# Kernel tuning notes

Hardware: AMD Instinct MI355X
Metric: run time of the kernel (lower is better)

## Reference

```python
import jax, jax.numpy as jnp
import numpy as np

B, N, D, G = 32, 1024, 512, 32  # batch, set size, in_features, num_gaussians


def setup_inputs() -> dict:
    key = jax.random.key(0)
    k1, k2 = jax.random.split(key)
    minibatch = jax.random.normal(k1, (B, N, D), dtype=jnp.float32)
    # xavier_uniform for Linear(D -> G)
    limit = float(np.sqrt(6.0 / (D + G)))
    W_pi = jax.random.uniform(k2, (G, D), dtype=jnp.float32, minval=-limit, maxval=limit)
    b_pi = jnp.zeros((G,), dtype=jnp.float32)
    return {"minibatch": minibatch, "W_pi": W_pi, "b_pi": b_pi}


def reference(minibatch, W_pi, b_pi):
    d = minibatch.shape[-1]
    o = d // 2
    # mixture weights per (batch, sample): softmax over gaussian axis
    logits = jnp.einsum('bnd,gd->bng', minibatch, W_pi) + b_pi  # [B,N,G]
    pi = jax.nn.softmax(logits, axis=2)
    mu = minibatch[:, :, :o]        # [B,N,O]
    sigma = minibatch[:, :, -o:]    # [B,N,O]
    weights = jnp.mean(pi, axis=1)  # [B,G]
    denom = jnp.sum(pi, axis=1)     # [B,G]
    # weighted first moment -> locs (vectorized over all gaussians at once)
    m1 = jnp.einsum('bng,bno->bgo', pi, mu)                 # [B,G,O]
    locs = m1 / denom[:, :, None]                            # [B,G,O]
    # weighted E[mu^2 + sigma^2]; variance = E[mu^2+sigma^2] - locs^2
    # (identical math to sum(pi*((locs-mu)^2 + sigma^2))/sum(pi))
    m2 = jnp.einsum('bng,bno->bgo', pi, mu * mu + sigma * sigma)
    var = m2 / denom[:, :, None] - locs * locs
    scales = jnp.sqrt(jnp.maximum(var, 0.0))                 # [B,G,O]
    return weights, scales, locs
```

## Files before the change

### kernel.cpp

```cpp
#include <hip/hip_runtime.h>
#include <stdint.h>

#define B_ 32
#define N_ 1024
#define D_ 512
#define G_ 32

typedef __attribute__((ext_vector_type(8))) short short8;
typedef __attribute__((ext_vector_type(4))) float f32x4;

union U4S8 { uint4 u; short8 s; };

#define WS_M   524288
#define WS_DN  2621440

__device__ inline uint32_t pack_bf16x2(float a, float b) {
  uint32_t ua = __float_as_uint(a);
  uint32_t ub = __float_as_uint(b);
  ua += 0x7FFFu + ((ua >> 16) & 1u);
  ub += 0x7FFFu + ((ub >> 16) & 1u);
  return (ua >> 16) | (ub & 0xFFFF0000u);
}
__device__ inline uint16_t bf16r(float a) {
  uint32_t u = __float_as_uint(a);
  u += 0x7FFFu + ((u >> 16) & 1u);
  return (uint16_t)(u >> 16);
}

__global__ __launch_bounds__(512, 8) void mdn_k1(
    const float* __restrict__ x, const float* __restrict__ W,
    const float* __restrict__ bpi, float* ws)
{
  __shared__ uint32_t Xb[4096];
  __shared__ uint32_t Wb[2048];
  __shared__ float SP[64 * 36];
  __shared__ uint32_t SPTb[1024];
  __shared__ float wpart[8 * 32];
  __shared__ float bias_s[G_];

  const int t = threadIdx.x;
  const int bid = blockIdx.x;
  const int b = bid >> 4;
  const int n0 = (bid & 15) * 64;
  const int wave = t >> 6;
  const int lane = t & 63;
  const int Mt = wave >> 1;
  const int Nt = wave & 1;

  int xr[2], xd[2];
  #pragma unroll
  for (int p = 0; p < 2; ++p) {
    int st = (p * 512 + t) * 16;
    xr[p] = st >> 8;
    xd[p] = ((st & 255) ^ ((xr[p] & 7) << 4)) >> 1;
  }
  int wg, wd;
  { int st = t * 16; wg = st >> 8; wd = ((st & 255) ^ ((wg & 7) << 4)) >> 1; }

  const float* xbase = x + ((size_t)b * N_ + n0) * D_;

  float4 fx[2][2], fw[2];
  #pragma unroll
  for (int p = 0; p < 2; ++p) {
    const float* s = xbase + xr[p] * D_ + xd[p];
    fx[p][0] = *(const float4*)s; fx[p][1] = *(const float4*)(s + 4);
  }
  { const float* s = W + wg * D_ + wd;
    fw[0] = *(const float4*)s; fw[1] = *(const float4*)(s + 4); }

  if (t < G_) bias_s[t] = bpi[t];

  f32x4 acc = {0.f, 0.f, 0.f, 0.f};

  #pragma unroll
  for (int dc = 0; dc < 4; ++dc) {
    #pragma unroll
    for (int p = 0; p < 2; ++p) {
      uint4 v;
      v.x = pack_bf16x2(fx[p][0].x, fx[p][0].y); v.y = pack_bf16x2(fx[p][0].z, fx[p][0].w);
      v.z = pack_bf16x2(fx[p][1].x, fx[p][1].y); v.w = pack_bf16x2(fx[p][1].z, fx[p][1].w);
      *(uint4*)((char*)Xb + (p * 512 + t) * 16) = v;
    }
    {
      uint4 v;
      v.x = pack_bf16x2(fw[0].x, fw[0].y); v.y = pack_bf16x2(fw[0].z, fw[0].w);
      v.z = pack_bf16x2(fw[1].x, fw[1].y); v.w = pack_bf16x2(fw[1].z, fw[1].w);
      *(uint4*)((char*)Wb + t * 16) = v;
    }
    __syncthreads();
    if (dc < 3) {
      #pragma unroll
      for (int p = 0; p < 2; ++p) {
        const float* s = xbase + xr[p] * D_ + (dc + 1) * 128 + xd[p];
        fx[p][0] = *(const float4*)s; fx[p][1] = *(const float4*)(s + 4);
      }
      const float* s = W + wg * D_ + (dc + 1) * 128 + wd;
      fw[0] = *(const float4*)s; fw[1] = *(const float4*)(s + 4);
    }
    #pragma unroll
    for (int ks = 0; ks < 4; ++ks) {
      int rowx = Mt * 16 + (lane & 15);
      int bytex = rowx * 256 + (((ks * 64) + ((lane >> 4) * 16)) ^ ((rowx & 7) << 4));
      short8 afr = *(short8*)((char*)Xb + bytex);
      int g = Nt * 16 + (lane & 15);
      int bytew = g * 256 + (((ks * 64) + ((lane >> 4) * 16)) ^ ((g & 7) << 4));
      short8 bfr = *(short8*)((char*)Wb + bytew);
      acc = __builtin_amdgcn_mfma_f32_16x16x32_bf16(afr, bfr, acc, 0, 0, 0);
    }
    __syncthreads();
  }

  {
    int g = Nt * 16 + (lane & 15);
    float bs = bias_s[g];
    int rbase = Mt * 16 + (lane >> 4) * 4;
    #pragma unroll
    for (int j = 0; j < 4; ++j) SP[(rbase + j) * 36 + g] = acc[j] + bs;
  }
  __syncthreads();

  {
    int r = t >> 3, gq = t & 7;
    float4 v = *(float4*)(SP + r * 36 + gq * 4);
    float m = fmaxf(fmaxf(v.x, v.y), fmaxf(v.z, v.w));
    m = fmaxf(m, __shfl_xor(m, 1));
    m = fmaxf(m, __shfl_xor(m, 2));
    m = fmaxf(m, __shfl_xor(m, 4));
    v.x = __expf(v.x - m); v.y = __expf(v.y - m);
    v.z = __expf(v.z - m); v.w = __expf(v.w - m);
    float s = v.x + v.y + v.z + v.w;
    s += __shfl_xor(s, 1); s += __shfl_xor(s, 2); s += __shfl_xor(s, 4);
    float inv = 1.0f / s;
    v.x *= inv; v.y *= inv; v.z *= inv; v.w *= inv;
    uint16_t* sp16 = (uint16_t*)SPTb;
    sp16[(gq * 4 + 0) * 64 + r] = bf16r(v.x);
    sp16[(gq * 4 + 1) * 64 + r] = bf16r(v.y);
    sp16[(gq * 4 + 2) * 64 + r] = bf16r(v.z);
    sp16[(gq * 4 + 3) * 64 + r] = bf16r(v.w);
    #pragma unroll
    for (int msk = 8; msk <= 32; msk <<= 1) {
      v.x += __shfl_xor(v.x, msk); v.y += __shfl_xor(v.y, msk);
      v.z += __shfl_xor(v.z, msk); v.w += __shfl_xor(v.w, msk);
    }
    if (lane < 8) {
      wpart[wave * 32 + lane * 4 + 0] = v.x;
      wpart[wave * 32 + lane * 4 + 1] = v.y;
      wpart[wave * 32 + lane * 4 + 2] = v.z;
      wpart[wave * 32 + lane * 4 + 3] = v.w;
    }
  }
  __syncthreads();

  if (t < 256) {
    int g = t >> 3, s = t & 7;
    uint4 v = *(uint4*)(SPTb + g * 32 + s * 4);
    *(uint4*)((uint32_t*)ws + (size_t)(b * 32 + g) * 512 + (n0 >> 1) + s * 4) = v;
  }
  if (t < G_) {
    float ssum = 0.f;
    #pragma unroll
    for (int w = 0; w < 8; ++w) ssum += wpart[w * 32 + t];
    ws[WS_DN + bid * 32 + t] = ssum;
  }
}

__global__ __launch_bounds__(512, 8) void mdn_k2(
    const float* __restrict__ x, float* ws)
{
  __shared__ uint32_t PT[32 * 132];
  __shared__ uint32_t XT[32 * 132];

  const int t = threadIdx.x;
  const int bid = blockIdx.x;
  const int b = bid >> 4;
  const int kc = (bid >> 2) & 3;
  const int q = bid & 3;
  const int wave = t >> 6, lane = t & 63;
  const int ot = wave;
  const int n0 = kc * 256;

  const uint32_t* piT = (const uint32_t*)ws;
  const int pg = t >> 4, psl = t & 15;
  const uint32_t* pbase = piT + (size_t)(b * 32 + pg) * 512 + kc * 128;
  uint4 pv0 = *(const uint4*)(pbase + psl * 4);
  uint4 pv1 = *(const uint4*)(pbase + (psl + 16) * 4);

  const int r2l = t >> 4, c4 = t & 15;
  const float* xb2 = x + ((size_t)b * N_ + n0) * D_ + q * 64 + 4 * c4;
  float4 a0, a1, sv0, sv1;
  {
    const float* s = xb2 + (size_t)(2 * r2l) * D_;
    a0 = *(const float4*)s;        a1 = *(const float4*)(s + D_);
    sv0 = *(const float4*)(s + 256); sv1 = *(const float4*)(s + D_ + 256);
  }

  *(uint4*)(PT + pg * 132 + psl * 4) = pv0;
  *(uint4*)(PT + pg * 132 + (psl + 16) * 4) = pv1;
  __syncthreads();

  f32x4 acc[2] = {{0.f,0.f,0.f,0.f},{0.f,0.f,0.f,0.f}};

  #pragma unroll
  for (int sc = 0; sc < 4; ++sc) {
    {
      uint4 wmu, wm2;
      wmu.x = pack_bf16x2(a0.x, a1.x); wmu.y = pack_bf16x2(a0.y, a1.y);
      wmu.z = pack_bf16x2(a0.z, a1.z); wmu.w = pack_bf16x2(a0.w, a1.w);
      float4 u0 = make_float4(fmaf(a0.x, a0.x, sv0.x * sv0.x), fmaf(a0.y, a0.y, sv0.y * sv0.y),
                              fmaf(a0.z, a0.z, sv0.z * sv0.z), fmaf(a0.w, a0.w, sv0.w * sv0.w));
      float4 u1 = make_float4(fmaf(a1.x, a1.x, sv1.x * sv1.x), fmaf(a1.y, a1.y, sv1.y * sv1.y),
                              fmaf(a1.z, a1.z, sv1.z * sv1.z), fmaf(a1.w, a1.w, sv1.w * sv1.w));
      wm2.x = pack_bf16x2(u0.x, u1.x); wm2.y = pack_bf16x2(u0.y, u1.y);
      wm2.z = pack_bf16x2(u0.z, u1.z); wm2.w = pack_bf16x2(u0.w, u1.w);
      *(uint4*)(XT + r2l * 132 + 4 * c4) = wmu;
      *(uint4*)(XT + r2l * 132 + 64 + 4 * c4) = wm2;
    }
    __syncthreads();
    if (sc < 3) {
      const float* s = xb2 + (size_t)((sc + 1) * 64 + 2 * r2l) * D_;
      a0 = *(const float4*)s;        a1 = *(const float4*)(s + D_);
      sv0 = *(const float4*)(s + 256); sv1 = *(const float4*)(s + D_ + 256);
    }
    #pragma unroll
    for (int kl = 0; kl < 2; ++kl) {
      int rb = kl * 16 + (lane >> 4) * 4;
      int ol = ot * 16 + (lane & 15);
      U4S8 bf;
      bf.u.x = XT[(rb + 0) * 132 + ol];
      bf.u.y = XT[(rb + 1) * 132 + ol];
      bf.u.z = XT[(rb + 2) * 132 + ol];
      bf.u.w = XT[(rb + 3) * 132 + ol];
      int r0h = (sc * 2 + kl) * 16 + (lane >> 4) * 4;
      #pragma unroll
      for (int gt = 0; gt < 2; ++gt) {
        int ga = gt * 16 + (lane & 15);
        short8 af = *(short8*)((char*)PT + (ga * 132 + r0h) * 4);
        acc[gt] = __builtin_amdgcn_mfma_f32_16x16x32_bf16(af, bf.s, acc[gt], 0, 0, 0);
      }
    }
    __syncthreads();
  }

  float* dst = ws + WS_M + (size_t)bid * 4096;
  #pragma unroll
  for (int gt = 0; gt < 2; ++gt) {
    int gout = gt * 16 + (lane >> 4) * 4;
    int col = ot * 16 + (lane & 15);
    #pragma unroll
    for (int j = 0; j < 4; ++j) dst[(gout + j) * 128 + col] = acc[gt][j];
  }
}

__global__ __launch_bounds__(256) void mdn_k3(
    const float* __restrict__ ws, float* __restrict__ out)
{
  __shared__ float dnm[G_];
  const int blk = blockIdx.x;
  const int b = blk >> 3, oc = blk & 7;
  const int t = threadIdx.x;
  if (t < G_) {
    float s = 0.f;
    #pragma unroll
    for (int c = 0; c < 16; ++c) s += ws[WS_DN + (b * 16 + c) * 32 + t];
    dnm[t] = s;
    if (oc == 0) out[b * G_ + t] = s * (1.0f / 1024.0f);
  }
  __syncthreads();
  const int g = t >> 3;
  const int o = oc * 32 + (t & 7) * 4;
  const int q = o >> 6;
  const int col = o & 63;
  float4 m1 = make_float4(0.f, 0.f, 0.f, 0.f);
  float4 m2 = make_float4(0.f, 0.f, 0.f, 0.f);
  #pragma unroll
  for (int kc = 0; kc < 4; ++kc) {
    const float* p = ws + WS_M + (size_t)((b * 16 + kc * 4 + q)) * 4096 + g * 128;
    float4 a = *(const float4*)(p + col);
    float4 c2 = *(const float4*)(p + 64 + col);
    m1.x += a.x; m1.y += a.y; m1.z += a.z; m1.w += a.w;
    m2.x += c2.x; m2.y += c2.y; m2.z += c2.z; m2.w += c2.w;
  }
  float inv = 1.0f / dnm[g];
  float4 lc = make_float4(m1.x * inv, m1.y * inv, m1.z * inv, m1.w * inv);
  float4 sc;
  sc.x = sqrtf(fmaxf(m2.x * inv - lc.x * lc.x, 0.f));
  sc.y = sqrtf(fmaxf(m2.y * inv - lc.y * lc.y, 0.f));
  sc.z = sqrtf(fmaxf(m2.z * inv - lc.z * lc.z, 0.f));
  sc.w = sqrtf(fmaxf(m2.w * inv - lc.w * lc.w, 0.f));
  float* scales = out + 1024;
  float* locs = out + 1024 + 262144;
  int oi = ((b * G_ + g) << 8) + o;
  *(float4*)(scales + oi) = sc;
  *(float4*)(locs + oi) = lc;
}

extern "C" void kernel_launch(void* const* d_in, const int* in_sizes, int n_in,
                              void* d_out, int out_size, void* d_ws, size_t ws_size,
                              hipStream_t stream)
{
  const float* x = (const float*)d_in[0];
  const float* W = (const float*)d_in[1];
  const float* bpi = (const float*)d_in[2];
  float* out = (float*)d_out;
  float* ws = (float*)d_ws;
  hipLaunchKernelGGL(mdn_k1, dim3(512), dim3(512), 0, stream, x, W, bpi, ws);
  hipLaunchKernelGGL(mdn_k2, dim3(512), dim3(512), 0, stream, x, ws);
  hipLaunchKernelGGL(mdn_k3, dim3(256), dim3(256), 0, stream, ws, out);
}
```

Baseline: 35.40 us.

## Load MFMA operands directly from global memory, dropping LDS staging in both GEMM kernels

Both GEMM kernels now run 256 threads instead of 512. Each wave loads its A and B fragments straight from global memory into registers and no longer stages X tiles through shared memory with barriers. In k1 each wave owns 16 rows and all 32 gaussians, so the softmax runs in registers via lane shuffles instead of through an LDS round trip. In k2 the pi fragments and the strided mu/sigma columns are read directly, trading LDS traffic and syncs for less coalesced scalar global loads and higher register pressure.

Result: slower. 37.45 us (+5.8%).

```diff
diff --git a/kernel.cpp b/kernel.cpp
--- a/kernel.cpp
+++ b/kernel.cpp
@@ -8,7 +8,6 @@
 
 typedef __attribute__((ext_vector_type(8))) short short8;
 typedef __attribute__((ext_vector_type(4))) float f32x4;
-
 union U4S8 { uint4 u; short8 s; };
 
 #define WS_M   524288
@@ -27,227 +26,171 @@
   return (uint16_t)(u >> 16);
 }
 
-__global__ __launch_bounds__(512, 8) void mdn_k1(
+__global__ __launch_bounds__(256, 2) void mdn_k1(
     const float* __restrict__ x, const float* __restrict__ W,
     const float* __restrict__ bpi, float* ws)
 {
-  __shared__ uint32_t Xb[4096];
-  __shared__ uint32_t Wb[2048];
-  __shared__ float SP[64 * 36];
-  __shared__ uint32_t SPTb[1024];
-  __shared__ float wpart[8 * 32];
-  __shared__ float bias_s[G_];
+  __shared__ uint32_t Wb[8192];
+  __shared__ uint32_t SPT[1024];
+  __shared__ float wpart[4][32];
 
   const int t = threadIdx.x;
   const int bid = blockIdx.x;
   const int b = bid >> 4;
   const int n0 = (bid & 15) * 64;
-  const int wave = t >> 6;
+  const int w = t >> 6;
   const int lane = t & 63;
-  const int Mt = wave >> 1;
-  const int Nt = wave & 1;
-
-  int xr[2], xd[2];
-  #pragma unroll
-  for (int p = 0; p < 2; ++p) {
-    int st = (p * 512 + t) * 16;
-    xr[p] = st >> 8;
-    xd[p] = ((st & 255) ^ ((xr[p] & 7) << 4)) >> 1;
-  }
-  int wg, wd;
-  { int st = t * 16; wg = st >> 8; wd = ((st & 255) ^ ((wg & 7) << 4)) >> 1; }
-
-  const float* xbase = x + ((size_t)b * N_ + n0) * D_;
-
-  float4 fx[2][2], fw[2];
-  #pragma unroll
-  for (int p = 0; p < 2; ++p) {
-    const float* s = xbase + xr[p] * D_ + xd[p];
-    fx[p][0] = *(const float4*)s; fx[p][1] = *(const float4*)(s + 4);
-  }
-  { const float* s = W + wg * D_ + wd;
-    fw[0] = *(const float4*)s; fw[1] = *(const float4*)(s + 4); }
-
-  if (t < G_) bias_s[t] = bpi[t];
-
-  f32x4 acc = {0.f, 0.f, 0.f, 0.f};
-
-  #pragma unroll
-  for (int dc = 0; dc < 4; ++dc) {
-    #pragma unroll
-    for (int p = 0; p < 2; ++p) {
-      uint4 v;
-      v.x = pack_bf16x2(fx[p][0].x, fx[p][0].y); v.y = pack_bf16x2(fx[p][0].z, fx[p][0].w);
-      v.z = pack_bf16x2(fx[p][1].x, fx[p][1].y); v.w = pack_bf16x2(fx[p][1].z, fx[p][1].w);
-      *(uint4*)((char*)Xb + (p * 512 + t) * 16) = v;
-    }
-    {
-      uint4 v;
-      v.x = pack_bf16x2(fw[0].x, fw[0].y); v.y = pack_bf16x2(fw[0].z, fw[0].w);
-      v.z = pack_bf16x2(fw[1].x, fw[1].y); v.w = pack_bf16x2(fw[1].z, fw[1].w);
-      *(uint4*)((char*)Wb + t * 16) = v;
-    }
-    __syncthreads();
-    if (dc < 3) {
-      #pragma unroll
-      for (int p = 0; p < 2; ++p) {
-        const float* s = xbase + xr[p] * D_ + (dc + 1) * 128 + xd[p];
-        fx[p][0] = *(const float4*)s; fx[p][1] = *(const float4*)(s + 4);
-      }
-      const float* s = W + wg * D_ + (dc + 1) * 128 + wd;
-      fw[0] = *(const float4*)s; fw[1] = *(const float4*)(s + 4);
-    }
-    #pragma unroll
-    for (int ks = 0; ks < 4; ++ks) {
-      int rowx = Mt * 16 + (lane & 15);
-      int bytex = rowx * 256 + (((ks * 64) + ((lane >> 4) * 16)) ^ ((rowx & 7) << 4));
-      short8 afr = *(short8*)((char*)Xb + bytex);
-      int g = Nt * 16 + (lane & 15);
-      int bytew = g * 256 + (((ks * 64) + ((lane >> 4) * 16)) ^ ((g & 7) << 4));
-      short8 bfr = *(short8*)((char*)Wb + bytew);
-      acc = __builtin_amdgcn_mfma_f32_16x16x32_bf16(afr, bfr, acc, 0, 0, 0);
-    }
-    __syncthreads();
-  }
-
-  {
-    int g = Nt * 16 + (lane & 15);
-    float bs = bias_s[g];
-    int rbase = Mt * 16 + (lane >> 4) * 4;
-    #pragma unroll
-    for (int j = 0; j < 4; ++j) SP[(rbase + j) * 36 + g] = acc[j] + bs;
+
+  #pragma unroll
+  for (int i = 0; i < 8; ++i) {
+    int s = t + i * 256;
+    int g = s >> 6;
+    int d0 = (s & 63) * 8;
+    const float4* src = (const float4*)(W + g * D_ + d0);
+    float4 f0 = src[0], f1 = src[1];
+    int ks = d0 >> 5, ksub = (d0 >> 3) & 3;
+    uint4 v;
+    v.x = pack_bf16x2(f0.x, f0.y); v.y = pack_bf16x2(f0.z, f0.w);
+    v.z = pack_bf16x2(f1.x, f1.y); v.w = pack_bf16x2(f1.z, f1.w);
+    *(uint4*)(Wb + (size_t)(((ks * 4 + ksub) * 32 + g) * 4)) = v;
   }
   __syncthreads();
 
-  {
-    int r = t >> 3, gq = t & 7;
-    float4 v = *(float4*)(SP + r * 36 + gq * 4);
-    float m = fmaxf(fmaxf(v.x, v.y), fmaxf(v.z, v.w));
+  const float* abase =
+      x + ((size_t)(b * N_ + n0 + w * 16 + (lane & 15))) * D_ + (lane >> 4) * 8;
+
+  f32x4 acc0 = {0.f, 0.f, 0.f, 0.f};
+  f32x4 acc1 = {0.f, 0.f, 0.f, 0.f};
+
+  float4 fa[16], fb[16];
+  #pragma unroll
+  for (int ks = 0; ks < 16; ++ks) {
+    fa[ks] = *(const float4*)(abase + ks * 32);
+    fb[ks] = *(const float4*)(abase + ks * 32 + 4);
+  }
+  #pragma unroll
+  for (int ks = 0; ks < 16; ++ks) {
+    U4S8 a;
+    a.u.x = pack_bf16x2(fa[ks].x, fa[ks].y);
+    a.u.y = pack_bf16x2(fa[ks].z, fa[ks].w);
+    a.u.z = pack_bf16x2(fb[ks].x, fb[ks].y);
+    a.u.w = pack_bf16x2(fb[ks].z, fb[ks].w);
+    int idx = ((ks * 4 + (lane >> 4)) * 32 + (lane & 15)) * 4;
+    U4S8 w0, w1;
+    w0.u = *(uint4*)(Wb + idx);
+    w1.u = *(uint4*)(Wb + idx + 64);
+    acc0 = __builtin_amdgcn_mfma_f32_16x16x32_bf16(a.s, w0.s, acc0, 0, 0, 0);
+    acc1 = __builtin_amdgcn_mfma_f32_16x16x32_bf16(a.s, w1.s, acc1, 0, 0, 0);
+  }
+
+  float bs0 = bpi[lane & 15], bs1 = bpi[16 + (lane & 15)];
+  float pi0[4], pi1[4];
+  float dsum0 = 0.f, dsum1 = 0.f;
+  #pragma unroll
+  for (int j = 0; j < 4; ++j) {
+    float v0 = acc0[j] + bs0, v1 = acc1[j] + bs1;
+    float m = fmaxf(v0, v1);
     m = fmaxf(m, __shfl_xor(m, 1));
     m = fmaxf(m, __shfl_xor(m, 2));
     m = fmaxf(m, __shfl_xor(m, 4));
-    v.x = __expf(v.x - m); v.y = __expf(v.y - m);
-    v.z = __expf(v.z - m); v.w = __expf(v.w - m);
-    float s = v.x + v.y + v.z + v.w;
-    s += __shfl_xor(s, 1); s += __shfl_xor(s, 2); s += __shfl_xor(s, 4);
+    m = fmaxf(m, __shfl_xor(m, 8));
+    float e0 = __expf(v0 - m), e1 = __expf(v1 - m);
+    float s = e0 + e1;
+    s += __shfl_xor(s, 1); s += __shfl_xor(s, 2);
+    s += __shfl_xor(s, 4); s += __shfl_xor(s, 8);
     float inv = 1.0f / s;
-    v.x *= inv; v.y *= inv; v.z *= inv; v.w *= inv;
-    uint16_t* sp16 = (uint16_t*)SPTb;
-    sp16[(gq * 4 + 0) * 64 + r] = bf16r(v.x);
-    sp16[(gq * 4 + 1) * 64 + r] = bf16r(v.y);
-    sp16[(gq * 4 + 2) * 64 + r] = bf16r(v.z);
-    sp16[(gq * 4 + 3) * 64 + r] = bf16r(v.w);
+    pi0[j] = e0 * inv; pi1[j] = e1 * inv;
+    dsum0 += pi0[j];   dsum1 += pi1[j];
+  }
+  dsum0 += __shfl_xor(dsum0, 16); dsum0 += __shfl_xor(dsum0, 32);
+  dsum1 += __shfl_xor(dsum1, 16); dsum1 += __shfl_xor(dsum1, 32);
+  if (lane < 16) { wpart[w][lane] = dsum0; wpart[w][16 + lane] = dsum1; }
+
+  {
+    uint16_t* sp16 = (uint16_t*)SPT;
+    int rl = w * 16 + (lane >> 4) * 4;
     #pragma unroll
-    for (int msk = 8; msk <= 32; msk <<= 1) {
-      v.x += __shfl_xor(v.x, msk); v.y += __shfl_xor(v.y, msk);
-      v.z += __shfl_xor(v.z, msk); v.w += __shfl_xor(v.w, msk);
+    for (int j = 0; j < 4; ++j) {
+      sp16[(lane & 15) * 64 + rl + j] = bf16r(pi0[j]);
+      sp16[(16 + (lane & 15)) * 64 + rl + j] = bf16r(pi1[j]);
     }
-    if (lane < 8) {
-      wpart[wave * 32 + lane * 4 + 0] = v.x;
-      wpart[wave * 32 + lane * 4 + 1] = v.y;
-      wpart[wave * 32 + lane * 4 + 2] = v.z;
-      wpart[wave * 32 + lane * 4 + 3] = v.w;
-    }
   }
   __syncthreads();
 
-  if (t < 256) {
-    int g = t >> 3, s = t & 7;
-    uint4 v = *(uint4*)(SPTb + g * 32 + s * 4);
-    *(uint4*)((uint32_t*)ws + (size_t)(b * 32 + g) * 512 + (n0 >> 1) + s * 4) = v;
-  }
-  if (t < G_) {
-    float ssum = 0.f;
-    #pragma unroll
-    for (int w = 0; w < 8; ++w) ssum += wpart[w * 32 + t];
-    ws[WS_DN + bid * 32 + t] = ssum;
-  }
-}
-
-__global__ __launch_bounds__(512, 8) void mdn_k2(
+  {
+    int g = t >> 3, i = t & 7;
+    uint4 v = *(uint4*)(SPT + g * 32 + i * 4);
+    *(uint4*)((uint32_t*)ws + (size_t)(b * 32 + g) * 512 + (n0 >> 1) + i * 4) = v;
+  }
+  if (t < 32) {
+    float s = wpart[0][t] + wpart[1][t] + wpart[2][t] + wpart[3][t];
+    ws[WS_DN + bid * 32 + t] = s;
+  }
+}
+
+__global__ __launch_bounds__(256, 2) void mdn_k2(
     const float* __restrict__ x, float* ws)
 {
-  __shared__ uint32_t PT[32 * 132];
-  __shared__ uint32_t XT[32 * 132];
-
   const int t = threadIdx.x;
   const int bid = blockIdx.x;
   const int b = bid >> 4;
   const int kc = (bid >> 2) & 3;
   const int q = bid & 3;
-  const int wave = t >> 6, lane = t & 63;
-  const int ot = wave;
-  const int n0 = kc * 256;
+  const int w = t >> 6;
+  const int lane = t & 63;
 
   const uint32_t* piT = (const uint32_t*)ws;
-  const int pg = t >> 4, psl = t & 15;
-  const uint32_t* pbase = piT + (size_t)(b * 32 + pg) * 512 + kc * 128;
-  uint4 pv0 = *(const uint4*)(pbase + psl * 4);
-  uint4 pv1 = *(const uint4*)(pbase + (psl + 16) * 4);
-
-  const int r2l = t >> 4, c4 = t & 15;
-  const float* xb2 = x + ((size_t)b * N_ + n0) * D_ + q * 64 + 4 * c4;
-  float4 a0, a1, sv0, sv1;
-  {
-    const float* s = xb2 + (size_t)(2 * r2l) * D_;
-    a0 = *(const float4*)s;        a1 = *(const float4*)(s + D_);
-    sv0 = *(const float4*)(s + 256); sv1 = *(const float4*)(s + D_ + 256);
-  }
-
-  *(uint4*)(PT + pg * 132 + psl * 4) = pv0;
-  *(uint4*)(PT + pg * 132 + (psl + 16) * 4) = pv1;
-  __syncthreads();
-
-  f32x4 acc[2] = {{0.f,0.f,0.f,0.f},{0.f,0.f,0.f,0.f}};
-
-  #pragma unroll
-  for (int sc = 0; sc < 4; ++sc) {
-    {
-      uint4 wmu, wm2;
-      wmu.x = pack_bf16x2(a0.x, a1.x); wmu.y = pack_bf16x2(a0.y, a1.y);
-      wmu.z = pack_bf16x2(a0.z, a1.z); wmu.w = pack_bf16x2(a0.w, a1.w);
-      float4 u0 = make_float4(fmaf(a0.x, a0.x, sv0.x * sv0.x), fmaf(a0.y, a0.y, sv0.y * sv0.y),
-                              fmaf(a0.z, a0.z, sv0.z * sv0.z), fmaf(a0.w, a0.w, sv0.w * sv0.w));
-      float4 u1 = make_float4(fmaf(a1.x, a1.x, sv1.x * sv1.x), fmaf(a1.y, a1.y, sv1.y * sv1.y),
-                              fmaf(a1.z, a1.z, sv1.z * sv1.z), fmaf(a1.w, a1.w, sv1.w * sv1.w));
-      wm2.x = pack_bf16x2(u0.x, u1.x); wm2.y = pack_bf16x2(u0.y, u1.y);
-      wm2.z = pack_bf16x2(u0.z, u1.z); wm2.w = pack_bf16x2(u0.w, u1.w);
-      *(uint4*)(XT + r2l * 132 + 4 * c4) = wmu;
-      *(uint4*)(XT + r2l * 132 + 64 + 4 * c4) = wm2;
+  const uint32_t* pa0 =
+      piT + (size_t)(b * 32 + (lane & 15)) * 512 + kc * 128 + (lane >> 4) * 4;
+  const uint32_t* pa1 = pa0 + 16 * 512;
+
+  const int ocol = q * 64 + w * 16 + (lane & 15);
+  const float* xb =
+      x + ((size_t)(b * N_) + kc * 256 + (lane >> 4) * 8) * D_ + ocol;
+
+  f32x4 aM10 = {0.f,0.f,0.f,0.f}, aM11 = {0.f,0.f,0.f,0.f};
+  f32x4 aM20 = {0.f,0.f,0.f,0.f}, aM21 = {0.f,0.f,0.f,0.f};
+
+  #pragma unroll
+  for (int ks = 0; ks < 8; ++ks) {
+    U4S8 A0, A1;
+    A0.u = *(const uint4*)(pa0 + ks * 16);
+    A1.u = *(const uint4*)(pa1 + ks * 16);
+    const float* xp = xb + (size_t)ks * 32 * D_;
+    float mu[8], sg[8];
+    #pragma unroll
+    for (int i = 0; i < 8; ++i) {
+      mu[i] = xp[i * D_];
+      sg[i] = xp[i * D_ + 256];
     }
-    __syncthreads();
-    if (sc < 3) {
-      const float* s = xb2 + (size_t)((sc + 1) * 64 + 2 * r2l) * D_;
-      a0 = *(const float4*)s;        a1 = *(const float4*)(s + D_);
-      sv0 = *(const float4*)(s + 256); sv1 = *(const float4*)(s + D_ + 256);
-    }
-    #pragma unroll
-    for (int kl = 0; kl < 2; ++kl) {
-      int rb = kl * 16 + (lane >> 4) * 4;
-      int ol = ot * 16 + (lane & 15);
-      U4S8 bf;
-      bf.u.x = XT[(rb + 0) * 132 + ol];
-      bf.u.y = XT[(rb + 1) * 132 + ol];
-      bf.u.z = XT[(rb + 2) * 132 + ol];
-      bf.u.w = XT[(rb + 3) * 132 + ol];
-      int r0h = (sc * 2 + kl) * 16 + (lane >> 4) * 4;
-      #pragma unroll
-      for (int gt = 0; gt < 2; ++gt) {
-        int ga = gt * 16 + (lane & 15);
-        short8 af = *(short8*)((char*)PT + (ga * 132 + r0h) * 4);
-        acc[gt] = __builtin_amdgcn_mfma_f32_16x16x32_bf16(af, bf.s, acc[gt], 0, 0, 0);
-      }
-    }
-    __syncthreads();
+    U4S8 Bm, B2;
+    Bm.u.x = pack_bf16x2(mu[0], mu[1]); Bm.u.y = pack_bf16x2(mu[2], mu[3]);
+    Bm.u.z = pack_bf16x2(mu[4], mu[5]); Bm.u.w = pack_bf16x2(mu[6], mu[7]);
+    float u0 = fmaf(mu[0], mu[0], sg[0] * sg[0]);
+    float u1 = fmaf(mu[1], mu[1], sg[1] * sg[1]);
+    float u2 = fmaf(mu[2], mu[2], sg[2] * sg[2]);
+    float u3 = fmaf(mu[3], mu[3], sg[3] * sg[3]);
+    float u4 = fmaf(mu[4], mu[4], sg[4] * sg[4]);
+    float u5 = fmaf(mu[5], mu[5], sg[5] * sg[5]);
+    float u6 = fmaf(mu[6], mu[6], sg[6] * sg[6]);
+    float u7 = fmaf(mu[7], mu[7], sg[7] * sg[7]);
+    B2.u.x = pack_bf16x2(u0, u1); B2.u.y = pack_bf16x2(u2, u3);
+    B2.u.z = pack_bf16x2(u4, u5); B2.u.w = pack_bf16x2(u6, u7);
+    aM10 = __builtin_amdgcn_mfma_f32_16x16x32_bf16(A0.s, Bm.s, aM10, 0, 0, 0);
+    aM11 = __builtin_amdgcn_mfma_f32_16x16x32_bf16(A1.s, Bm.s, aM11, 0, 0, 0);
+    aM20 = __builtin_amdgcn_mfma_f32_16x16x32_bf16(A0.s, B2.s, aM20, 0, 0, 0);
+    aM21 = __builtin_amdgcn_mfma_f32_16x16x32_bf16(A1.s, B2.s, aM21, 0, 0, 0);
   }
 
   float* dst = ws + WS_M + (size_t)bid * 4096;
-  #pragma unroll
-  for (int gt = 0; gt < 2; ++gt) {
-    int gout = gt * 16 + (lane >> 4) * 4;
-    int col = ot * 16 + (lane & 15);
-    #pragma unroll
-    for (int j = 0; j < 4; ++j) dst[(gout + j) * 128 + col] = acc[gt][j];
+  const int cl = w * 16 + (lane & 15);
+  #pragma unroll
+  for (int j = 0; j < 4; ++j) {
+    int g0 = (lane >> 4) * 4 + j;
+    dst[g0 * 128 + cl] = aM10[j];
+    dst[(16 + g0) * 128 + cl] = aM11[j];
+    dst[g0 * 128 + 64 + cl] = aM20[j];
+    dst[(16 + g0) * 128 + 64 + cl] = aM21[j];
   }
 }
 
@@ -303,7 +246,7 @@
   const float* bpi = (const float*)d_in[2];
   float* out = (float*)d_out;
   float* ws = (float*)d_ws;
-  hipLaunchKernelGGL(mdn_k1, dim3(512), dim3(512), 0, stream, x, W, bpi, ws);
-  hipLaunchKernelGGL(mdn_k2, dim3(512), dim3(512), 0, stream, x, ws);
+  hipLaunchKernelGGL(mdn_k1, dim3(512), dim3(256), 0, stream, x, W, bpi, ws);
+  hipLaunchKernelGGL(mdn_k2, dim3(512), dim3(256), 0, stream, x, ws);
   hipLaunchKernelGGL(mdn_k3, dim3(256), dim3(256), 0, stream, ws, out);
 }
```
